# Optimization experiments

Hardware: AMD Instinct MI355X
Metric: run time of the kernel (lower is better)

The kernel has to match this reference:

```python
import jax, jax.numpy as jnp
import numpy as np

T = 16          # timesteps
BATCH = 8       # video clips -> leading dim of x is BATCH*T = 128
C_IN = 768      # fixed by nn.Conv2d(768, redu_dim, 1)
D = 256         # redu_dim
K = 64          # num_centers
H = W = 28
EPS = 1e-12     # torch F.normalize eps


def _conv(x, w, padding):
    # x: [N,C,H,W], w: [O,I,kh,kw]
    return jax.lax.conv_general_dilated(
        x, w, window_strides=(1, 1), padding=padding,
        dimension_numbers=('NCHW', 'OIHW', 'NCHW'))


def setup_inputs() -> dict:
    key = jax.random.key(0)
    ks = jax.random.split(key, 9)
    x = jax.random.normal(ks[0], (BATCH * T, C_IN, H, W), dtype=jnp.float32)
    redu_w = jax.random.normal(ks[1], (D, C_IN, 1, 1), jnp.float32) * 0.02
    redu_b = jnp.zeros((D,), jnp.float32)
    share_w = jax.random.normal(ks[2], (K, D, 1, 1), jnp.float32) * 0.05
    share_b = jnp.zeros((K,), jnp.float32)
    U_z = jax.random.normal(ks[3], (K, K, 3, 3), jnp.float32) * 0.04
    U_r = jax.random.normal(ks[4], (K, K, 3, 3), jnp.float32) * 0.04
    U_h = jax.random.normal(ks[5], (K, K, 3, 3), jnp.float32) * 0.04
    centers = jax.random.normal(ks[6], (K, D), jnp.float32) * 0.06
    return {"x": x, "redu_w": redu_w, "redu_b": redu_b,
            "share_w": share_w, "share_b": share_b,
            "U_z": U_z, "U_r": U_r, "U_h": U_h,
            "centers": centers, "timesteps": T}


def reference(x, redu_w, redu_b, share_w, share_b, U_z, U_r, U_h, centers, timesteps):
    t = timesteps
    bt, _, h, w = x.shape
    b = bt // t
    k = share_w.shape[0]
    d = redu_w.shape[0]

    # channel reduction (1x1 conv)
    xr = _conv(x, redu_w, 'VALID') + redu_b[None, :, None, None]        # [bt,d,h,w]
    # shared assignment logits (1x1 conv)
    wxb = _conv(xr, share_w, 'VALID') + share_b[None, :, None, None]     # [bt,k,h,w]
    wxb = wxb.reshape(b, t, k, h, w).transpose(1, 0, 2, 3, 4)            # [t,b,k,h,w]

    # sequential ConvGRU over timesteps
    h0 = jnp.zeros((b, k, h, w), x.dtype)
    def step(h_tm1, w_t):
        z = jax.nn.sigmoid(w_t + _conv(h_tm1, U_z, 'SAME'))
        r = jax.nn.sigmoid(w_t + _conv(h_tm1, U_r, 'SAME'))
        hh = jnp.tanh(w_t + _conv(r * h_tm1, U_h, 'SAME'))
        h_new = (1.0 - z) * hh + z * h_tm1
        return h_new, h_new
    _, hs = jax.lax.scan(step, h0, wxb)                                  # [t,b,k,h,w]

    assign = hs.transpose(1, 0, 2, 3, 4).reshape(b * t, k, h * w)        # [bt,k,hw]
    # softmax over centers per spatial location
    assign = jax.nn.softmax(assign, axis=1)

    # VLAD aggregation
    a_sum = assign.sum(axis=-1, keepdims=True)                           # [bt,k,1]
    a = a_sum * centers[None]                                            # [bt,k,d]
    xf = xr.reshape(b * t, d, h * w)                                     # [bt,d,hw]
    vlad = jnp.einsum('bkp,bdp->bkd', assign, xf) - a                    # [bt,k,d]

    vlad = vlad.reshape(b, t, k, d).sum(axis=1)                          # [b,k,d]
    # intra-norm over feature dim, then global L2 norm
    vlad = vlad / jnp.maximum(jnp.linalg.norm(vlad, axis=2, keepdims=True), EPS)
    vlad = vlad.reshape(b, k * d)
    vlad = vlad / jnp.maximum(jnp.linalg.norm(vlad, axis=1, keepdims=True), EPS)
    return vlad
```

## Files before the change

kernel.cpp:

```cpp
#include <hip/hip_runtime.h>
#include <hip/hip_bf16.h>

#define T_ 16
#define B_ 8
#define CIN 768
#define D_ 256
#define K_ 64
#define HW 784
#define W_ 28

typedef short short8 __attribute__((ext_vector_type(8)));
typedef short short4v __attribute__((ext_vector_type(4)));
typedef float floatx4 __attribute__((ext_vector_type(4)));
typedef unsigned short ushort_t;

__device__ __forceinline__ unsigned short f2bf(float x) {
    union { float f; unsigned u; } v; v.f = x;
    unsigned u = v.u;
    unsigned r = (u + 0x7fffu + ((u >> 16) & 1u)) >> 16;
    return (unsigned short)r;
}
__device__ __forceinline__ float bf2f(unsigned short h) {
    union { unsigned u; float f; } v; v.u = ((unsigned)h) << 16; return v.f;
}

__device__ __forceinline__ float block_reduce_sum_256(float v) {
    for (int off = 32; off > 0; off >>= 1) v += __shfl_down(v, off, 64);
    __shared__ float red[4];
    __shared__ float tot;
    int lane = threadIdx.x & 63, wid = threadIdx.x >> 6;
    if (lane == 0) red[wid] = v;
    __syncthreads();
    if (threadIdx.x == 0) tot = red[0] + red[1] + red[2] + red[3];
    __syncthreads();
    return tot;
}

__global__ __launch_bounds__(256) void cvt_weights(
    const float* __restrict__ rw, const float* __restrict__ sw,
    const float* __restrict__ Uz, const float* __restrict__ Ur,
    const float* __restrict__ Uh,
    ushort_t* __restrict__ whi, ushort_t* __restrict__ wlo,
    ushort_t* __restrict__ shi, ushort_t* __restrict__ slo,
    ushort_t* __restrict__ azh, ushort_t* __restrict__ azl,
    ushort_t* __restrict__ ahh, ushort_t* __restrict__ ahl)
{
    int i = blockIdx.x * 256 + threadIdx.x;
    const int nR = D_ * CIN;
    const int nS = K_ * D_;
    const int nZR = 128 * 576;
    const int nH = 64 * 576;
    if (i < nR) {
        float x = rw[i];
        unsigned short h = f2bf(x);
        whi[i] = h; wlo[i] = f2bf(x - bf2f(h));
    } else if (i < nR + nS) {
        int j = i - nR;
        float x = sw[j];
        unsigned short h = f2bf(x);
        shi[j] = h; slo[j] = f2bf(x - bf2f(h));
    } else if (i < nR + nS + nZR) {
        int j = i - nR - nS;
        int row = j / 576, kk = j - row * 576;
        int tap = kk >> 6, c = kk & 63;
        const float* U = (row < 64) ? Uz : Ur;
        float x = U[(((size_t)(row & 63)) * 64 + c) * 9 + tap];
        unsigned short h = f2bf(x);
        azh[j] = h; azl[j] = f2bf(x - bf2f(h));
    } else if (i < nR + nS + nZR + nH) {
        int j = i - nR - nS - nZR;
        int row = j / 576, kk = j - row * 576;
        int tap = kk >> 6, c = kk & 63;
        float x = Uh[(((size_t)row) * 64 + c) * 9 + tap];
        unsigned short h = f2bf(x);
        ahh[j] = h; ahl[j] = f2bf(x - bf2f(h));
    }
}

template<int BM, int THR, int KD>
__global__ __launch_bounds__(THR, 4) void mfma_conv1x1(
    const float* __restrict__ X, const ushort_t* __restrict__ Whi,
    const ushort_t* __restrict__ Wlo, const float* __restrict__ bias,
    float* __restrict__ Out)
{
    const int nt = blockIdx.x, bt = blockIdx.z;
    const int p0 = nt * 112;
    const int tid = threadIdx.x, lane = tid & 63, wv = tid >> 6;
    const int li = lane & 15, koff = (lane >> 4) * 8;
    constexpr int NWAVE = THR / 64;
    constexpr int MI = BM / (NWAVE * 16);
    constexpr int NKS = KD / 32;
    constexpr int UPT = (THR == 512) ? 1 : 2;
    const float* Xb = X + (size_t)bt * KD * HW;
    float* Ob = Out + (size_t)bt * BM * HW;

    __shared__ ushort_t lB[2][2][112 * 40];

    floatx4 acc[MI][7];
#pragma unroll
    for (int a = 0; a < MI; ++a)
#pragma unroll
        for (int b = 0; b < 7; ++b) acc[a][b] = (floatx4){0.f, 0.f, 0.f, 0.f};

    float bA[8 * UPT], bB[8 * UPT];
    short8 ahi[MI], alo[MI];

    auto loadB = [&](int k0, float* bb) {
#pragma unroll
        for (int u = 0; u < UPT; ++u) {
            int uu = tid + u * THR;
            if (uu < 448) {
                int j = uu / 112, pp = uu - j * 112;
                const float* xp = Xb + (size_t)(k0 + j * 8) * HW + p0 + pp;
#pragma unroll
                for (int c = 0; c < 8; ++c) bb[u * 8 + c] = xp[(size_t)c * HW];
            }
        }
    };
    auto writeB = [&](const float* bb, int wb) {
#pragma unroll
        for (int u = 0; u < UPT; ++u) {
            int uu = tid + u * THR;
            if (uu < 448) {
                int j = uu / 112, pp = uu - j * 112;
                short8 vh, vl;
#pragma unroll
                for (int c = 0; c < 8; ++c) {
                    unsigned short h = f2bf(bb[u * 8 + c]);
                    vh[c] = (short)h; vl[c] = (short)f2bf(bb[u * 8 + c] - bf2f(h));
                }
                *(short8*)&lB[wb][0][pp * 40 + j * 8] = vh;
                *(short8*)&lB[wb][1][pp * 40 + j * 8] = vl;
            }
        }
    };
    auto loadA = [&](int k0) {
#pragma unroll
        for (int mi = 0; mi < MI; ++mi) {
            int m = wv * (MI * 16) + mi * 16 + li;
            ahi[mi] = *(const short8*)(Whi + (size_t)m * KD + k0 + koff);
            alo[mi] = *(const short8*)(Wlo + (size_t)m * KD + k0 + koff);
        }
    };
    auto domfma = [&](int rb) {
        const ushort_t* bh = &lB[rb][0][0];
        const ushort_t* bl = &lB[rb][1][0];
#pragma unroll
        for (int ni = 0; ni < 7; ++ni) {
            int n = ni * 16 + li;
            short8 bhi = *(const short8*)&bh[n * 40 + koff];
            short8 blo = *(const short8*)&bl[n * 40 + koff];
#pragma unroll
            for (int mi = 0; mi < MI; ++mi) {
                acc[mi][ni] = __builtin_amdgcn_mfma_f32_16x16x32_bf16(ahi[mi], bhi, acc[mi][ni], 0, 0, 0);
                acc[mi][ni] = __builtin_amdgcn_mfma_f32_16x16x32_bf16(ahi[mi], blo, acc[mi][ni], 0, 0, 0);
                acc[mi][ni] = __builtin_amdgcn_mfma_f32_16x16x32_bf16(alo[mi], bhi, acc[mi][ni], 0, 0, 0);
            }
        }
    };

    loadB(0, bA);
    writeB(bA, 0);
    loadB(32, bB);
    __syncthreads();

    for (int ks = 0; ks < NKS; ks += 2) {
        loadA(ks * 32);
        if (ks + 1 < NKS) writeB(bB, 1);
        if (ks + 2 < NKS) loadB((ks + 2) * 32, bA);
        domfma(0);
        __syncthreads();
        loadA((ks + 1) * 32);
        if (ks + 2 < NKS) writeB(bA, 0);
        if (ks + 3 < NKS) loadB((ks + 3) * 32, bB);
        domfma(1);
        __syncthreads();
    }

#pragma unroll
    for (int mi = 0; mi < MI; ++mi) {
        int m0g = wv * (MI * 16) + mi * 16 + ((lane >> 4) << 2);
#pragma unroll
        for (int ni = 0; ni < 7; ++ni) {
            int p = p0 + ni * 16 + li;
#pragma unroll
            for (int r = 0; r < 4; ++r)
                Ob[(size_t)(m0g + r) * HW + p] = acc[mi][ni][r] + bias[m0g + r];
        }
    }
}

__global__ __launch_bounds__(512, 2) void gru_step(
    const ushort_t* __restrict__ hRhi, const ushort_t* __restrict__ hRlo,
    ushort_t* __restrict__ hWhi, ushort_t* __restrict__ hWlo,
    const ushort_t* __restrict__ azh, const ushort_t* __restrict__ azl,
    const ushort_t* __restrict__ ahh, const ushort_t* __restrict__ ahl,
    const float* __restrict__ wxb, float* __restrict__ hs_t, int t)
{
    const int y0 = blockIdx.x, b = blockIdx.y;
    const int tid = threadIdx.x, lane = tid & 63, wv = tid >> 6;
    const int li = lane & 15, koff8 = (lane >> 4) * 8, kq = (lane >> 4) * 4;

    __shared__ ushort_t Hhi[5 * 30 * 72], Hlo[5 * 30 * 72];
    __shared__ ushort_t Rhi[3 * 30 * 72], Rlo[3 * 30 * 72];
    __shared__ float zs[28 * 68];

    {
        const ushort_t* gh = hRhi + (size_t)b * HW * 64;
        const ushort_t* gl = hRlo + (size_t)b * HW * 64;
        for (int e = tid; e < 1200; e += 512) {
            int r = e / 240, rem = e - r * 240;
            int lx = rem >> 3, j = rem & 7;
            int gy = y0 - 2 + r, gx = lx - 1;
            short8 vh = {0,0,0,0,0,0,0,0}, vl = {0,0,0,0,0,0,0,0};
            if (gy >= 0 && gy < 28 && gx >= 0 && gx < 28) {
                size_t go = ((size_t)(gy * 28 + gx)) * 64 + j * 8;
                vh = *(const short8*)(gh + go);
                vl = *(const short8*)(gl + go);
            }
            int lo = (r * 30 + lx) * 72 + j * 8;
            *(short8*)&Hhi[lo] = vh;
            *(short8*)&Hlo[lo] = vl;
        }
        short8 z8 = {0,0,0,0,0,0,0,0};
        for (int e = tid; e < 1620; e += 512) {
            if (e < 810) *(short8*)&Rhi[e * 8] = z8;
            else         *(short8*)&Rlo[(e - 810) * 8] = z8;
        }
    }
    __syncthreads();

    const float* wx = wxb + ((size_t)(b * T_ + t) * K_) * HW;
    const int c0 = li;
    const int c1 = (li < 12) ? 16 + li : 0;

    if (wv < 4) {
        const int kb = wv * 16;
        const ushort_t* Ah = azh + (size_t)(kb + li) * 576;
        const ushort_t* Al = azl + (size_t)(kb + li) * 576;
        floatx4 az[2];
        az[0] = (floatx4){0.f,0.f,0.f,0.f}; az[1] = (floatx4){0.f,0.f,0.f,0.f};
#pragma unroll
        for (int tap = 0; tap < 9; ++tap) {
            const int dy = tap / 3, dx = tap - dy * 3;
#pragma unroll
            for (int ch = 0; ch < 2; ++ch) {
                short8 whi_ = *(const short8*)(Ah + tap * 64 + ch * 32 + koff8);
                short8 wlo_ = *(const short8*)(Al + tap * 64 + ch * 32 + koff8);
                int cb = ch * 32 + koff8;
                int o0 = ((dy + 1) * 30 + c0 + dx) * 72 + cb;
                int o1 = ((dy + 1) * 30 + c1 + dx) * 72 + cb;
                short8 bh0 = *(const short8*)&Hhi[o0];
                short8 bl0 = *(const short8*)&Hlo[o0];
                short8 bh1 = *(const short8*)&Hhi[o1];
                short8 bl1 = *(const short8*)&Hlo[o1];
                az[0] = __builtin_amdgcn_mfma_f32_16x16x32_bf16(whi_, bh0, az[0], 0, 0, 0);
                az[0] = __builtin_amdgcn_mfma_f32_16x16x32_bf16(whi_, bl0, az[0], 0, 0, 0);
                az[0] = __builtin_amdgcn_mfma_f32_16x16x32_bf16(wlo_, bh0, az[0], 0, 0, 0);
                az[1] = __builtin_amdgcn_mfma_f32_16x16x32_bf16(whi_, bh1, az[1], 0, 0, 0);
                az[1] = __builtin_amdgcn_mfma_f32_16x16x32_bf16(whi_, bl1, az[1], 0, 0, 0);
                az[1] = __builtin_amdgcn_mfma_f32_16x16x32_bf16(wlo_, bh1, az[1], 0, 0, 0);
            }
        }
        const int kb4 = kb + kq;
#pragma unroll
        for (int cf = 0; cf < 2; ++cf) {
            int c = cf * 16 + li;
            if (c < 28) {
                floatx4 zv;
#pragma unroll
                for (int r = 0; r < 4; ++r)
                    zv[r] = 1.f / (1.f + __expf(-(wx[(size_t)(kb4 + r) * HW + y0 * 28 + c] + az[cf][r])));
                *(floatx4*)&zs[c * 68 + kb4] = zv;
            }
        }
    } else {
        const int kb = (wv - 4) * 16;
        const ushort_t* Ah = azh + (size_t)(64 + kb + li) * 576;
        const ushort_t* Al = azl + (size_t)(64 + kb + li) * 576;
        floatx4 ar[3][2];
#pragma unroll
        for (int i = 0; i < 3; ++i) {
            ar[i][0] = (floatx4){0.f,0.f,0.f,0.f};
            ar[i][1] = (floatx4){0.f,0.f,0.f,0.f};
        }
#pragma unroll
        for (int tap = 0; tap < 9; ++tap) {
            const int dy = tap / 3, dx = tap - dy * 3;
#pragma unroll
            for (int ch = 0; ch < 2; ++ch) {
                short8 whi_ = *(const short8*)(Ah + tap * 64 + ch * 32 + koff8);
                short8 wlo_ = *(const short8*)(Al + tap * 64 + ch * 32 + koff8);
                int cb = ch * 32 + koff8;
#pragma unroll
                for (int rr = 0; rr < 3; ++rr) {
                    int o0 = ((rr + dy) * 30 + c0 + dx) * 72 + cb;
                    int o1 = ((rr + dy) * 30 + c1 + dx) * 72 + cb;
                    short8 bh0 = *(const short8*)&Hhi[o0];
                    short8 bl0 = *(const short8*)&Hlo[o0];
                    short8 bh1 = *(const short8*)&Hhi[o1];
                    short8 bl1 = *(const short8*)&Hlo[o1];
                    ar[rr][0] = __builtin_amdgcn_mfma_f32_16x16x32_bf16(whi_, bh0, ar[rr][0], 0, 0, 0);
                    ar[rr][0] = __builtin_amdgcn_mfma_f32_16x16x32_bf16(whi_, bl0, ar[rr][0], 0, 0, 0);
                    ar[rr][0] = __builtin_amdgcn_mfma_f32_16x16x32_bf16(wlo_, bh0, ar[rr][0], 0, 0, 0);
                    ar[rr][1] = __builtin_amdgcn_mfma_f32_16x16x32_bf16(whi_, bh1, ar[rr][1], 0, 0, 0);
                    ar[rr][1] = __builtin_amdgcn_mfma_f32_16x16x32_bf16(whi_, bl1, ar[rr][1], 0, 0, 0);
                    ar[rr][1] = __builtin_amdgcn_mfma_f32_16x16x32_bf16(wlo_, bh1, ar[rr][1], 0, 0, 0);
                }
            }
        }
        const int kb4 = kb + kq;
#pragma unroll
        for (int rr = 0; rr < 3; ++rr) {
            int gy = y0 - 1 + rr;
            if (gy < 0 || gy >= 28) continue;
#pragma unroll
            for (int cf = 0; cf < 2; ++cf) {
                int c = cf * 16 + li;
                if (c >= 28) continue;
                short4v ph = *(const short4v*)&Hhi[((rr + 1) * 30 + c + 1) * 72 + kb4];
                short4v pl = *(const short4v*)&Hlo[((rr + 1) * 30 + c + 1) * 72 + kb4];
                short4v vh, vl;
#pragma unroll
                for (int r = 0; r < 4; ++r) {
                    float rv = 1.f / (1.f + __expf(-(wx[(size_t)(kb4 + r) * HW + gy * 28 + c] + ar[rr][cf][r])));
                    float hv = bf2f((unsigned short)ph[r]) + bf2f((unsigned short)pl[r]);
                    float rh = rv * hv;
                    unsigned short h = f2bf(rh);
                    vh[r] = (short)h; vl[r] = (short)f2bf(rh - bf2f(h));
                }
                *(short4v*)&Rhi[(rr * 30 + c + 1) * 72 + kb4] = vh;
                *(short4v*)&Rlo[(rr * 30 + c + 1) * 72 + kb4] = vl;
            }
        }
    }
    __syncthreads();

    if (wv < 4) {
        const int kb = wv * 16;
        const ushort_t* Ah = ahh + (size_t)(kb + li) * 576;
        const ushort_t* Al = ahl + (size_t)(kb + li) * 576;
        floatx4 ac[2];
        ac[0] = (floatx4){0.f,0.f,0.f,0.f}; ac[1] = (floatx4){0.f,0.f,0.f,0.f};
#pragma unroll
        for (int tap = 0; tap < 9; ++tap) {
            const int dy = tap / 3, dx = tap - dy * 3;
#pragma unroll
            for (int ch = 0; ch < 2; ++ch) {
                short8 whi_ = *(const short8*)(Ah + tap * 64 + ch * 32 + koff8);
                short8 wlo_ = *(const short8*)(Al + tap * 64 + ch * 32 + koff8);
                int cb = ch * 32 + koff8;
                int o0 = (dy * 30 + c0 + dx) * 72 + cb;
                int o1 = (dy * 30 + c1 + dx) * 72 + cb;
                short8 bh0 = *(const short8*)&Rhi[o0];
                short8 bl0 = *(const short8*)&Rlo[o0];
                short8 bh1 = *(const short8*)&Rhi[o1];
                short8 bl1 = *(const short8*)&Rlo[o1];
                ac[0] = __builtin_amdgcn_mfma_f32_16x16x32_bf16(whi_, bh0, ac[0], 0, 0, 0);
                ac[0] = __builtin_amdgcn_mfma_f32_16x16x32_bf16(whi_, bl0, ac[0], 0, 0, 0);
                ac[0] = __builtin_amdgcn_mfma_f32_16x16x32_bf16(wlo_, bh0, ac[0], 0, 0, 0);
                ac[1] = __builtin_amdgcn_mfma_f32_16x16x32_bf16(whi_, bh1, ac[1], 0, 0, 0);
                ac[1] = __builtin_amdgcn_mfma_f32_16x16x32_bf16(whi_, bl1, ac[1], 0, 0, 0);
                ac[1] = __builtin_amdgcn_mfma_f32_16x16x32_bf16(wlo_, bh1, ac[1], 0, 0, 0);
            }
        }
        const int kb4 = kb + kq;
        float* hsb = hs_t + (size_t)b * K_ * HW;
#pragma unroll
        for (int cf = 0; cf < 2; ++cf) {
            int c = cf * 16 + li;
            if (c >= 28) continue;
            int p = y0 * 28 + c;
            floatx4 zv = *(const floatx4*)&zs[c * 68 + kb4];
            short4v ph = *(const short4v*)&Hhi[(2 * 30 + c + 1) * 72 + kb4];
            short4v pl = *(const short4v*)&Hlo[(2 * 30 + c + 1) * 72 + kb4];
            short4v vh, vl;
#pragma unroll
            for (int r = 0; r < 4; ++r) {
                int k = kb4 + r;
                float xv = wx[(size_t)k * HW + p] + ac[cf][r];
                float e2 = __expf(2.f * xv);
                float th = 1.f - 2.f / (e2 + 1.f);
                float hp = bf2f((unsigned short)ph[r]) + bf2f((unsigned short)pl[r]);
                float hn = (1.f - zv[r]) * th + zv[r] * hp;
                hsb[(size_t)k * HW + p] = hn;
                unsigned short h = f2bf(hn);
                vh[r] = (short)h; vl[r] = (short)f2bf(hn - bf2f(h));
            }
            size_t o = ((size_t)(b * HW) + p) * 64 + kb4;
            *(short4v*)(hWhi + o) = vh;
            *(short4v*)(hWlo + o) = vl;
        }
    }
}

__global__ __launch_bounds__(256) void softmax_k(float* __restrict__ hs)
{
    int q = blockIdx.x;
    int py = blockIdx.y;
    float* base = hs + (size_t)q * K_ * HW;
    for (int p = py * 392 + threadIdx.x; p < (py + 1) * 392 && p < HW; p += 256) {
        float v[64];
        float m = -1e30f;
#pragma unroll
        for (int k = 0; k < 64; ++k) {
            v[k] = base[(size_t)k * HW + p];
            m = fmaxf(m, v[k]);
        }
        float s = 0.f;
#pragma unroll
        for (int k = 0; k < 64; ++k) {
            v[k] = __expf(v[k] - m);
            s += v[k];
        }
        float inv = 1.f / s;
#pragma unroll
        for (int k = 0; k < 64; ++k)
            base[(size_t)k * HW + p] = v[k] * inv;
    }
}

__global__ __launch_bounds__(256) void vlad_k(const float* __restrict__ assign,
    const float* __restrict__ xr, float* __restrict__ vladt,
    float* __restrict__ asum_bt)
{
    int dt = blockIdx.x, t = blockIdx.y, b = blockIdx.z;
    int q = t * B_ + b, bt = b * T_ + t, d0 = dt * 64;
    const float* ab = assign + (size_t)q * K_ * HW;
    const float* xb = xr + (size_t)bt * D_ * HW;
    __shared__ float As[16][68];
    __shared__ float Xs[16][68];
    int tx = threadIdx.x & 15, ty = threadIdx.x >> 4;
    float acc[4][4] = {{0.f}};
    float pacc[4] = {0.f, 0.f, 0.f, 0.f};

    for (int p0 = 0; p0 < HW; p0 += 16) {
#pragma unroll
        for (int it = 0; it < 4; ++it) {
            int e = threadIdx.x + it * 256;
            int row = e >> 4, pp = e & 15;
            float av_ = ab[(size_t)row * HW + p0 + pp];
            As[pp][row] = av_;
            if (dt == 0) pacc[it] += av_;
            Xs[pp][row] = xb[(size_t)(d0 + row) * HW + p0 + pp];
        }
        __syncthreads();
#pragma unroll
        for (int pp = 0; pp < 16; ++pp) {
            float4 a = *(const float4*)&As[pp][ty * 4];
            float4 xv = *(const float4*)&Xs[pp][tx * 4];
            float av[4] = {a.x, a.y, a.z, a.w};
            float xvv[4] = {xv.x, xv.y, xv.z, xv.w};
#pragma unroll
            for (int r = 0; r < 4; ++r)
#pragma unroll
                for (int s = 0; s < 4; ++s)
                    acc[r][s] = fmaf(av[r], xvv[s], acc[r][s]);
        }
        __syncthreads();
    }
#pragma unroll
    for (int r = 0; r < 4; ++r) {
        int k = ty * 4 + r;
        float4 o = {acc[r][0], acc[r][1], acc[r][2], acc[r][3]};
        *(float4*)&vladt[((size_t)bt * K_ + k) * D_ + d0 + tx * 4] = o;
    }
    if (dt == 0) {
#pragma unroll
        for (int it = 0; it < 4; ++it) {
            float s = pacc[it];
#pragma unroll
            for (int off = 1; off < 16; off <<= 1) s += __shfl_xor(s, off, 16);
            if (tx == 0) asum_bt[(size_t)bt * 64 + ty + it * 16] = s;
        }
    }
}

__global__ __launch_bounds__(256) void norm1_k(const float* __restrict__ vladt,
    const float* __restrict__ asum_bt, const float* __restrict__ centers,
    float* __restrict__ out)
{
    int bid = blockIdx.x; int b = bid >> 6, k = bid & 63; int d = threadIdx.x;
    float acc = 0.f;
#pragma unroll
    for (int t = 0; t < T_; ++t)
        acc += vladt[(((size_t)b * T_ + t) * K_ + k) * D_ + d];
    float asum = 0.f;
#pragma unroll
    for (int t = 0; t < T_; ++t)
        asum += asum_bt[(size_t)(b * T_ + t) * 64 + k];
    acc -= asum * centers[(size_t)k * D_ + d];
    float ss = block_reduce_sum_256(acc * acc);
    float n = fmaxf(sqrtf(ss), 1e-12f);
    out[((size_t)b * K_ + k) * D_ + d] = acc / n;
}

__global__ __launch_bounds__(256) void norm2_k(float* __restrict__ out)
{
    int b = blockIdx.x;
    float* v = out + (size_t)b * (K_ * D_);
    float s = 0.f;
    for (int i = threadIdx.x; i < K_ * D_; i += 256) {
        float x = v[i];
        s = fmaf(x, x, s);
    }
    float tot = block_reduce_sum_256(s);
    float n = fmaxf(sqrtf(tot), 1e-12f);
    for (int i = threadIdx.x; i < K_ * D_; i += 256) v[i] = v[i] / n;
}

extern "C" void kernel_launch(void* const* d_in, const int* in_sizes, int n_in,
                              void* d_out, int out_size, void* d_ws, size_t ws_size,
                              hipStream_t stream)
{
    const float* x       = (const float*)d_in[0];
    const float* redu_w  = (const float*)d_in[1];
    const float* redu_b  = (const float*)d_in[2];
    const float* share_w = (const float*)d_in[3];
    const float* share_b = (const float*)d_in[4];
    const float* Uz      = (const float*)d_in[5];
    const float* Ur      = (const float*)d_in[6];
    const float* Uh      = (const float*)d_in[7];
    const float* centers = (const float*)d_in[8];

    float* ws = (float*)d_ws;
    const size_t SZ_XR   = (size_t)128 * D_ * HW;
    const size_t SZ_WXB  = (size_t)128 * K_ * HW;
    const size_t SZ_HS   = (size_t)T_ * B_ * K_ * HW;
    const size_t SZ_PLANE= (size_t)B_ * K_ * HW;

    float* xr     = ws;
    float* wxb    = xr + SZ_XR;
    float* hs     = wxb + SZ_WXB;
    float* asum_bt= hs + SZ_HS;
    float* wsplit = asum_bt + 8192;
    float* area   = wsplit + 323584;

    ushort_t* whi = (ushort_t*)wsplit;
    ushort_t* wlo = whi + 196608;
    ushort_t* shi = wlo + 196608;
    ushort_t* slo = shi + 16384;
    ushort_t* azh = slo + 16384;
    ushort_t* azl = azh + 73728;
    ushort_t* ahh = azl + 73728;
    ushort_t* ahl = ahh + 36864;

    float* vladt = area;
    ushort_t* st = (ushort_t*)area;
    ushort_t* h0hi = st;
    ushort_t* h0lo = st + SZ_PLANE;
    ushort_t* h1hi = st + 2 * SZ_PLANE;
    ushort_t* h1lo = st + 3 * SZ_PLANE;

    hipMemsetAsync(h0hi, 0, 2 * SZ_PLANE * sizeof(ushort_t), stream);

    cvt_weights<<<dim3((D_ * CIN + K_ * D_ + 128 * 576 + 64 * 576 + 255) / 256),
                  256, 0, stream>>>(redu_w, share_w, Uz, Ur, Uh,
                                    whi, wlo, shi, slo, azh, azl, ahh, ahl);

    mfma_conv1x1<256, 512, CIN><<<dim3(7, 1, 128), 512, 0, stream>>>(x, whi, wlo, redu_b, xr);
    mfma_conv1x1<64, 256, D_><<<dim3(7, 1, 128), 256, 0, stream>>>(xr, shi, slo, share_b, wxb);

    for (int t = 0; t < T_; ++t) {
        const ushort_t* rh_ = (t & 1) ? h1hi : h0hi;
        const ushort_t* rl_ = (t & 1) ? h1lo : h0lo;
        ushort_t* wh_ = (t & 1) ? h0hi : h1hi;
        ushort_t* wl_ = (t & 1) ? h0lo : h1lo;
        gru_step<<<dim3(28, 8), 512, 0, stream>>>(rh_, rl_, wh_, wl_,
                                                  azh, azl, ahh, ahl,
                                                  wxb, hs + (size_t)t * SZ_PLANE, t);
    }

    softmax_k<<<dim3(128, 2), 256, 0, stream>>>(hs);

    vlad_k<<<dim3(4, 16, 8), 256, 0, stream>>>(hs, xr, vladt, asum_bt);
    norm1_k<<<512, 256, 0, stream>>>(vladt, asum_bt, centers, (float*)d_out);
    norm2_k<<<8, 256, 0, stream>>>((float*)d_out);
}
```

Baseline: 684.3 us.

## Split conv1x1 output channels across blocks and single-buffer the LDS tile

The first 1x1 conv kernel now uses 256-thread blocks that each compute 128 of the 256 output channels, so the grid doubles in the M dimension. The LDS tile becomes single-buffered (half the shared memory) with two barriers per k-step, and the register prefetch of the next tile is kept. The goal is more resident blocks and better occupancy. The cost is that each X tile is loaded and converted twice (once per M half), and the extra synchronisation weakens overlap between loads and MFMA.

```diff
diff --git a/kernel.cpp b/kernel.cpp
--- a/kernel.cpp
+++ b/kernel.cpp
@@ -77,24 +77,22 @@
     }
 }
 
-template<int BM, int THR, int KD>
-__global__ __launch_bounds__(THR, 4) void mfma_conv1x1(
+template<int MTOT, int BM, int KD, int MINW>
+__global__ __launch_bounds__(256, MINW) void mfma_conv1x1(
     const float* __restrict__ X, const ushort_t* __restrict__ Whi,
     const ushort_t* __restrict__ Wlo, const float* __restrict__ bias,
     float* __restrict__ Out)
 {
-    const int nt = blockIdx.x, bt = blockIdx.z;
-    const int p0 = nt * 112;
+    const int nt = blockIdx.x, mt = blockIdx.y, bt = blockIdx.z;
+    const int p0 = nt * 112, m0 = mt * BM;
     const int tid = threadIdx.x, lane = tid & 63, wv = tid >> 6;
     const int li = lane & 15, koff = (lane >> 4) * 8;
-    constexpr int NWAVE = THR / 64;
-    constexpr int MI = BM / (NWAVE * 16);
+    constexpr int MI = BM / 64;
     constexpr int NKS = KD / 32;
-    constexpr int UPT = (THR == 512) ? 1 : 2;
     const float* Xb = X + (size_t)bt * KD * HW;
-    float* Ob = Out + (size_t)bt * BM * HW;
-
-    __shared__ ushort_t lB[2][2][112 * 40];
+    float* Ob = Out + (size_t)bt * MTOT * HW;
+
+    __shared__ ushort_t lB[2][112 * 40];
 
     floatx4 acc[MI][7];
 #pragma unroll
@@ -102,54 +100,58 @@
 #pragma unroll
         for (int b = 0; b < 7; ++b) acc[a][b] = (floatx4){0.f, 0.f, 0.f, 0.f};
 
-    float bA[8 * UPT], bB[8 * UPT];
+    const int mbase = m0 + wv * (MI * 16);
+
+    const int u0j = tid / 112, u0p = tid - u0j * 112;
+    const bool u1v = tid < 192;
+    const int u1j = (tid + 256) / 112, u1p = (tid + 256) - u1j * 112;
+
+    float b0[16], b1[16];
     short8 ahi[MI], alo[MI];
 
     auto loadB = [&](int k0, float* bb) {
-#pragma unroll
-        for (int u = 0; u < UPT; ++u) {
-            int uu = tid + u * THR;
-            if (uu < 448) {
-                int j = uu / 112, pp = uu - j * 112;
-                const float* xp = Xb + (size_t)(k0 + j * 8) * HW + p0 + pp;
-#pragma unroll
-                for (int c = 0; c < 8; ++c) bb[u * 8 + c] = xp[(size_t)c * HW];
-            }
+        const float* xp0 = Xb + (size_t)(k0 + u0j * 8) * HW + p0 + u0p;
+#pragma unroll
+        for (int c = 0; c < 8; ++c) bb[c] = xp0[(size_t)c * HW];
+        if (u1v) {
+            const float* xp1 = Xb + (size_t)(k0 + u1j * 8) * HW + p0 + u1p;
+#pragma unroll
+            for (int c = 0; c < 8; ++c) bb[8 + c] = xp1[(size_t)c * HW];
         }
     };
-    auto writeB = [&](const float* bb, int wb) {
-#pragma unroll
-        for (int u = 0; u < UPT; ++u) {
-            int uu = tid + u * THR;
-            if (uu < 448) {
-                int j = uu / 112, pp = uu - j * 112;
-                short8 vh, vl;
-#pragma unroll
-                for (int c = 0; c < 8; ++c) {
-                    unsigned short h = f2bf(bb[u * 8 + c]);
-                    vh[c] = (short)h; vl[c] = (short)f2bf(bb[u * 8 + c] - bf2f(h));
-                }
-                *(short8*)&lB[wb][0][pp * 40 + j * 8] = vh;
-                *(short8*)&lB[wb][1][pp * 40 + j * 8] = vl;
-            }
+    auto writeB = [&](const float* bb) {
+        short8 vh, vl;
+#pragma unroll
+        for (int c = 0; c < 8; ++c) {
+            unsigned short h = f2bf(bb[c]);
+            vh[c] = (short)h; vl[c] = (short)f2bf(bb[c] - bf2f(h));
+        }
+        *(short8*)&lB[0][u0p * 40 + u0j * 8] = vh;
+        *(short8*)&lB[1][u0p * 40 + u0j * 8] = vl;
+        if (u1v) {
+#pragma unroll
+            for (int c = 0; c < 8; ++c) {
+                unsigned short h = f2bf(bb[8 + c]);
+                vh[c] = (short)h; vl[c] = (short)f2bf(bb[8 + c] - bf2f(h));
+            }
+            *(short8*)&lB[0][u1p * 40 + u1j * 8] = vh;
+            *(short8*)&lB[1][u1p * 40 + u1j * 8] = vl;
         }
     };
     auto loadA = [&](int k0) {
 #pragma unroll
         for (int mi = 0; mi < MI; ++mi) {
-            int m = wv * (MI * 16) + mi * 16 + li;
+            int m = mbase + mi * 16 + li;
             ahi[mi] = *(const short8*)(Whi + (size_t)m * KD + k0 + koff);
             alo[mi] = *(const short8*)(Wlo + (size_t)m * KD + k0 + koff);
         }
     };
-    auto domfma = [&](int rb) {
-        const ushort_t* bh = &lB[rb][0][0];
-        const ushort_t* bl = &lB[rb][1][0];
+    auto domfma = [&]() {
 #pragma unroll
         for (int ni = 0; ni < 7; ++ni) {
             int n = ni * 16 + li;
-            short8 bhi = *(const short8*)&bh[n * 40 + koff];
-            short8 blo = *(const short8*)&bl[n * 40 + koff];
+            short8 bhi = *(const short8*)&lB[0][n * 40 + koff];
+            short8 blo = *(const short8*)&lB[1][n * 40 + koff];
 #pragma unroll
             for (int mi = 0; mi < MI; ++mi) {
                 acc[mi][ni] = __builtin_amdgcn_mfma_f32_16x16x32_bf16(ahi[mi], bhi, acc[mi][ni], 0, 0, 0);
@@ -159,27 +161,25 @@
         }
     };
 
-    loadB(0, bA);
-    writeB(bA, 0);
-    loadB(32, bB);
-    __syncthreads();
-
+    loadB(0, b0);
     for (int ks = 0; ks < NKS; ks += 2) {
         loadA(ks * 32);
-        if (ks + 1 < NKS) writeB(bB, 1);
-        if (ks + 2 < NKS) loadB((ks + 2) * 32, bA);
-        domfma(0);
+        writeB(b0);
+        __syncthreads();
+        if (ks + 1 < NKS) loadB((ks + 1) * 32, b1);
+        domfma();
         __syncthreads();
         loadA((ks + 1) * 32);
-        if (ks + 2 < NKS) writeB(bA, 0);
-        if (ks + 3 < NKS) loadB((ks + 3) * 32, bB);
-        domfma(1);
+        writeB(b1);
         __syncthreads();
+        if (ks + 2 < NKS) loadB((ks + 2) * 32, b0);
+        domfma();
+        __syncthreads();
     }
 
 #pragma unroll
     for (int mi = 0; mi < MI; ++mi) {
-        int m0g = wv * (MI * 16) + mi * 16 + ((lane >> 4) << 2);
+        int m0g = mbase + mi * 16 + ((lane >> 4) << 2);
 #pragma unroll
         for (int ni = 0; ni < 7; ++ni) {
             int p = p0 + ni * 16 + li;
@@ -558,8 +558,8 @@
                   256, 0, stream>>>(redu_w, share_w, Uz, Ur, Uh,
                                     whi, wlo, shi, slo, azh, azl, ahh, ahl);
 
-    mfma_conv1x1<256, 512, CIN><<<dim3(7, 1, 128), 512, 0, stream>>>(x, whi, wlo, redu_b, xr);
-    mfma_conv1x1<64, 256, D_><<<dim3(7, 1, 128), 256, 0, stream>>>(xr, shi, slo, share_b, wxb);
+    mfma_conv1x1<256, 128, CIN, 3><<<dim3(7, 2, 128), 256, 0, stream>>>(x, whi, wlo, redu_b, xr);
+    mfma_conv1x1<64, 64, D_, 4><<<dim3(7, 1, 128), 256, 0, stream>>>(xr, shi, slo, share_b, wxb);
 
     for (int t = 0; t < T_; ++t) {
         const ushort_t* rh_ = (t & 1) ? h1hi : h0hi;
```

After: 654.7 us. -4.3%, faster.
